# Kernel optimization log

Hardware: AMD Instinct MI355X
Metric: run time of the kernel (lower is better)

Reference implementation:

```python
import jax, jax.numpy as jnp
import numpy as np

B, C, H, W = 16, 1024, 32, 32  # H*W must equal C (required by matmul(h, fg) in the source)
EPS = 1e-5
NEG_SLOPE = 0.01


def setup_inputs() -> dict:
    key = jax.random.key(0)
    ks = jax.random.split(key, 12)
    s = 1.0 / np.sqrt(C)
    inp = {"x": jax.random.normal(ks[0], (B, C, H, W), jnp.float32)}
    for i, name in enumerate(["f", "g", "h", "c"]):
        inp[f"W{name}"] = jax.random.normal(ks[1 + 2 * i], (C, C), jnp.float32) * s
        inp[f"b{name}"] = jax.random.normal(ks[2 + 2 * i], (C,), jnp.float32) * 0.01
    inp["gamma"] = jnp.ones((C,), jnp.float32)
    inp["beta"] = jnp.zeros((C,), jnp.float32)
    inp["rmean"] = jax.random.normal(ks[9], (C,), jnp.float32) * 0.01
    inp["rvar"] = jax.random.uniform(ks[10], (C,), jnp.float32, 0.5, 1.5)
    return inp


def reference(x, Wf, bf, Wg, bg, Wh, bh, Wc, bc, gamma, beta, rmean, rvar):
    b, c, h_, w_ = x.shape
    n = h_ * w_  # == c by construction
    xf = x.reshape(b, c, n)

    def proj(Wp, bp):  # 1x1 conv == per-pixel channel matmul
        return jnp.einsum('oc,bcn->bon', Wp, xf) + bp[None, :, None]

    f = proj(Wf, bf)              # (B, C, N)
    g = proj(Wg, bg)              # (B, C, N); transposed(1,2) handled in einsum
    hh = proj(Wh, bh)             # (B, C, N)
    scores = jnp.einsum('bcn,bdn->bcd', f, g)        # f @ g^T -> (B, C, C)
    attn = jax.nn.softmax(scores, axis=1)            # softmax over dim=1 (as in source)
    # dropout2d(p=0.5) is identity in eval mode
    hfg = jnp.einsum('bcn,bnd->bcd', hh, attn)       # matmul(h, fg), needs N == C
    hfg = hfg.reshape(b, c, h_, w_)
    y = jnp.einsum('oc,bchw->bohw', Wc, hfg) + bc[None, :, None, None]
    y = jnp.where(y >= 0, y, NEG_SLOPE * y)          # LeakyReLU
    inv = gamma / jnp.sqrt(rvar + EPS)               # BatchNorm (eval mode)
    y = (y - rmean[None, :, None, None]) * inv[None, :, None, None] + beta[None, :, None, None]
    return y + x
```

## Files before the change

### kernel.cpp

```cpp
#include <hip/hip_runtime.h>
#include <cstdint>
#include <cstddef>

using half8  = __attribute__((ext_vector_type(8))) _Float16;
using half4  = __attribute__((ext_vector_type(4))) _Float16;
using float4v = __attribute__((ext_vector_type(4))) float;

#define CD 1024
#define M2 (1024 * 1024)

#define GLD16(gp, lp)                                                          \
    __builtin_amdgcn_global_load_lds(                                          \
        (const __attribute__((address_space(1))) void*)(gp),                   \
        (__attribute__((address_space(3))) void*)(lp), 16, 0, 0)

__global__ void prep_weights(const float* __restrict__ Wf, const float* __restrict__ Wg,
                             const float* __restrict__ Wh, const float* __restrict__ Wc,
                             const float* __restrict__ bf, const float* __restrict__ bg,
                             const float* __restrict__ bh,
                             _Float16* __restrict__ Wfgh, _Float16* __restrict__ WcH,
                             float* __restrict__ bstack) {
    int idx = blockIdx.x * 256 + threadIdx.x;
    if (idx < 3 * M2) {
        const float* s = idx < M2 ? Wf : (idx < 2 * M2 ? Wg : Wh);
        int off = idx & (M2 - 1);
        Wfgh[idx] = (_Float16)s[off];
    } else if (idx < 4 * M2) {
        WcH[idx - 3 * M2] = (_Float16)Wc[idx - 3 * M2];
    } else if (idx < 4 * M2 + 3 * CD) {
        int j = idx - 4 * M2;
        const float* s = j < CD ? bf : (j < 2 * CD ? bg : bh);
        bstack[j] = s[j & (CD - 1)];
    }
}

__global__ void transpose_x(const float* __restrict__ x, _Float16* __restrict__ xT, int b0) {
    __shared__ float tile[32][33];
    int z = blockIdx.z;
    const float* xb = x + (size_t)(b0 + z) * M2;
    _Float16* xTb = xT + (size_t)z * M2;
    int n0 = blockIdx.x * 32, k0 = blockIdx.y * 32;
    int tx = threadIdx.x, ty = threadIdx.y;
#pragma unroll
    for (int i = 0; i < 4; i++)
        tile[ty + i * 8][tx] = xb[(size_t)(k0 + ty + i * 8) * CD + n0 + tx];
    __syncthreads();
#pragma unroll
    for (int i = 0; i < 4; i++)
        xTb[(size_t)(n0 + ty + i * 8) * CD + k0 + tx] = (_Float16)tile[tx][ty + i * 8];
}

__global__ __launch_bounds__(256) void gemv_bch(const float* __restrict__ Wc,
                                                const float* __restrict__ bh,
                                                float* __restrict__ bch) {
    int o = blockIdx.x * 4 + (threadIdx.x >> 6);
    int lane = threadIdx.x & 63;
    float s = 0.f;
    for (int c = lane; c < CD; c += 64) s += Wc[(size_t)o * CD + c] * bh[c];
#pragma unroll
    for (int off = 32; off > 0; off >>= 1) s += __shfl_xor(s, off);
    if (lane == 0) bch[o] = s;
}

__global__ __launch_bounds__(256) void gemm128(const _Float16* __restrict__ A,
                                               const _Float16* __restrict__ B,
                                               _Float16* __restrict__ C) {
    __shared__ __align__(16) _Float16 As[128][32];
    __shared__ __align__(16) _Float16 Bs[128][32];
    int row0 = blockIdx.y * 128, col0 = blockIdx.x * 128;
    int tid = threadIdx.x, lane = tid & 63, wave = tid >> 6;
    int wr = wave >> 1, wc = wave & 1;
    const int srow = lane >> 2;
    const int scol = (lane & 3) * 8;
    const size_t gA0 = (size_t)(row0 + wave * 16 + srow) * 1024 + scol;
    const size_t gA1 = gA0 + (size_t)64 * 1024;
    const size_t gB0 = (size_t)(col0 + wave * 16 + srow) * 1024 + scol;
    const size_t gB1 = gB0 + (size_t)64 * 1024;
    _Float16* ldsA0 = &As[wave * 16][0];
    _Float16* ldsA1 = &As[64 + wave * 16][0];
    _Float16* ldsB0 = &Bs[wave * 16][0];
    _Float16* ldsB1 = &Bs[64 + wave * 16][0];
    float4v acc[4][4] = {};
    const int kq = (lane >> 4) * 8, rl = lane & 15;
    for (int kt = 0; kt < 1024; kt += 32) {
        GLD16(A + gA0 + kt, ldsA0);
        GLD16(A + gA1 + kt, ldsA1);
        GLD16(B + gB0 + kt, ldsB0);
        GLD16(B + gB1 + kt, ldsB1);
        __syncthreads();
        half8 af[4], bfr[4];
#pragma unroll
        for (int m = 0; m < 4; m++) af[m] = *(const half8*)(&As[wr * 64 + m * 16 + rl][kq]);
#pragma unroll
        for (int n = 0; n < 4; n++) bfr[n] = *(const half8*)(&Bs[wc * 64 + n * 16 + rl][kq]);
#pragma unroll
        for (int m = 0; m < 4; m++)
#pragma unroll
            for (int n = 0; n < 4; n++)
                acc[m][n] = __builtin_amdgcn_mfma_f32_16x16x32_f16(af[m], bfr[n], acc[m][n], 0, 0, 0);
        __syncthreads();
    }
#pragma unroll
    for (int m = 0; m < 4; m++)
#pragma unroll
        for (int r = 0; r < 4; r++) {
            int row = row0 + wr * 64 + m * 16 + ((lane >> 4) << 2) + r;
#pragma unroll
            for (int n = 0; n < 4; n++) {
                int col = col0 + wc * 64 + n * 16 + (lane & 15);
                C[(size_t)row * 1024 + col] = (_Float16)acc[m][n][r];
            }
        }
}

__global__ __launch_bounds__(256) void softmax_col(const float* __restrict__ ST,
                                                   _Float16* __restrict__ attnT) {
    int d = blockIdx.x, z = blockIdx.y;
    const float* row = ST + ((size_t)z * CD + d) * CD;
    _Float16* orow = attnT + ((size_t)z * CD + d) * CD;
    int t = threadIdx.x;
    float4v v = *(const float4v*)(row + t * 4);
    float mx = fmaxf(fmaxf(v[0], v[1]), fmaxf(v[2], v[3]));
#pragma unroll
    for (int o = 32; o > 0; o >>= 1) mx = fmaxf(mx, __shfl_xor(mx, o));
    __shared__ float redm[4], reds[4];
    int wave = t >> 6, lane = t & 63;
    if (lane == 0) redm[wave] = mx;
    __syncthreads();
    mx = fmaxf(fmaxf(redm[0], redm[1]), fmaxf(redm[2], redm[3]));
    float e[4];
    float s = 0.f;
#pragma unroll
    for (int i = 0; i < 4; i++) {
        e[i] = __expf(v[i] - mx);
        s += e[i];
    }
#pragma unroll
    for (int o = 32; o > 0; o >>= 1) s += __shfl_xor(s, o);
    if (lane == 0) reds[wave] = s;
    __syncthreads();
    s = reds[0] + reds[1] + reds[2] + reds[3];
    float inv = 1.0f / s;
    half4 ov;
#pragma unroll
    for (int i = 0; i < 4; i++) ov[i] = (_Float16)(e[i] * inv);
    *(half4*)(orow + t * 4) = ov;
}

enum { EP_F16B = 0, EP_F32 = 1, EP_F16 = 2, EP_FIN = 3 };

#define STAGE_A(T, BUF)                                                        \
    GLD16(gA0 + (size_t)(T) * 32, &As[BUF][wv * 16][0]);                       \
    GLD16(gA1 + (size_t)(T) * 32, &As[BUF][128 + wv * 16][0]);
#define STAGE_B(T, BUF)                                                        \
    GLD16(gB0 + (size_t)(T) * 32, &Bs[BUF][wv * 16][0]);                       \
    GLD16(gB1 + (size_t)(T) * 32, &Bs[BUF][128 + wv * 16][0]);

#define TILE(BUF, DOSTAGE, STT, STBUF, VMSTR)                                  \
    {                                                                          \
        asm volatile("s_waitcnt " VMSTR ::: "memory");                         \
        __builtin_amdgcn_sched_barrier(0);                                     \
        __builtin_amdgcn_s_barrier();                                          \
        _Pragma("unroll") for (int m = 0; m < 4; m++)                          \
            a[m] = *(const half8*)&As[BUF][wr * 128 + m * 16 + rl][kqa];       \
        _Pragma("unroll") for (int n = 0; n < 4; n++)                          \
            b[n] = *(const half8*)&Bs[BUF][wc * 64 + n * 16 + rl][kqa];        \
        _Pragma("unroll") for (int m = 4; m < 8; m++)                          \
            a[m] = *(const half8*)&As[BUF][wr * 128 + m * 16 + rl][kqa];       \
        if (DOSTAGE) { STAGE_A(STT, STBUF) STAGE_B(STT, STBUF) }               \
        __builtin_amdgcn_sched_barrier(0);                                     \
        __builtin_amdgcn_s_setprio(1);                                         \
        _Pragma("unroll") for (int m = 0; m < 8; m++)                          \
            _Pragma("unroll") for (int n = 0; n < 4; n++)                      \
                acc[m][n] = __builtin_amdgcn_mfma_f32_16x16x32_f16(            \
                    a[m], b[n], acc[m][n], 0, 0, 0);                           \
        __builtin_amdgcn_s_setprio(0);                                         \
    }

template <int EPI>
__global__ __launch_bounds__(512, 2) void gemm_nt(
    const _Float16* __restrict__ A, int64_t sA, const _Float16* __restrict__ B, int64_t sB,
    void* __restrict__ Cp, int64_t sC, const float* __restrict__ bias,
    const float* __restrict__ bc, const float* __restrict__ gamma,
    const float* __restrict__ beta, const float* __restrict__ rmean,
    const float* __restrict__ rvar, const float* __restrict__ xres) {
    __shared__ __align__(16) _Float16 As[4][256][32];
    __shared__ __align__(16) _Float16 Bs[4][256][32];
    int z = blockIdx.z;
    const _Float16* Ab = A + (size_t)z * sA;
    const _Float16* Bb = B + (size_t)z * sB;
    int row0 = blockIdx.y * 256, col0 = blockIdx.x * 256;
    int tid = threadIdx.x, lane = tid & 63, wv = tid >> 6;
    int wr = wv >> 2, wc = wv & 3;

    const int srow = wv * 16 + (lane >> 2);
    const int scol = ((lane & 3) ^ ((lane >> 3) & 3)) * 8;
    const _Float16* gA0 = Ab + (size_t)(row0 + srow) * 1024 + scol;
    const _Float16* gA1 = gA0 + (size_t)128 * 1024;
    const _Float16* gB0 = Bb + (size_t)(col0 + srow) * 1024 + scol;
    const _Float16* gB1 = gB0 + (size_t)128 * 1024;

    const int rl = lane & 15;
    const int kq = (lane >> 4) * 8;
    const int kqa = kq ^ (((rl >> 1) & 3) << 3);

    float4v acc[8][4] = {};
    half8 a[8], b[4];

    STAGE_A(0, 0) STAGE_B(0, 0)
    STAGE_A(1, 1) STAGE_B(1, 1)
    STAGE_A(2, 2) STAGE_B(2, 2)

#pragma unroll 1
    for (int g = 0; g < 7; ++g) {
        int t = g * 4;
        TILE(0, 1, t + 3, 3, "vmcnt(8)")
        TILE(1, 1, t + 4, 0, "vmcnt(8)")
        TILE(2, 1, t + 5, 1, "vmcnt(8)")
        TILE(3, 1, t + 6, 2, "vmcnt(8)")
    }
    TILE(0, 1, 31, 3, "vmcnt(8)")
    TILE(1, 0, 0, 0, "vmcnt(8)")
    TILE(2, 0, 0, 0, "vmcnt(4)")
    TILE(3, 0, 0, 0, "vmcnt(0)")

#pragma unroll
    for (int m = 0; m < 8; m++) {
#pragma unroll
        for (int r = 0; r < 4; r++) {
            int row = row0 + wr * 128 + m * 16 + ((lane >> 4) << 2) + r;
            float add0 = 0.f, mu = 0.f, invs = 1.f, bet = 0.f;
            if constexpr (EPI == EP_F16B) add0 = bias[row];
            if constexpr (EPI == EP_FIN) {
                add0 = bc[row];
                mu = rmean[row];
                invs = gamma[row] * rsqrtf(rvar[row] + 1e-5f);
                bet = beta[row];
            }
#pragma unroll
            for (int n = 0; n < 4; n++) {
                int col = col0 + wc * 64 + n * 16 + (lane & 15);
                float v = acc[m][n][r];
                if constexpr (EPI == EP_F16B) {
                    ((_Float16*)Cp)[(size_t)z * sC + (size_t)row * 1024 + col] = (_Float16)(v + add0);
                } else if constexpr (EPI == EP_F32) {
                    ((float*)Cp)[(size_t)z * sC + (size_t)row * 1024 + col] = v;
                } else if constexpr (EPI == EP_F16) {
                    ((_Float16*)Cp)[(size_t)z * sC + (size_t)row * 1024 + col] = (_Float16)v;
                } else {
                    v += add0;
                    v = v >= 0.f ? v : 0.01f * v;
                    v = (v - mu) * invs + bet;
                    v += xres[(size_t)z * M2 + (size_t)row * 1024 + col];
                    ((float*)Cp)[(size_t)z * sC + (size_t)row * 1024 + col] = v;
                }
            }
        }
    }
}

extern "C" void kernel_launch(void* const* d_in, const int* in_sizes, int n_in,
                              void* d_out, int out_size, void* d_ws, size_t ws_size,
                              hipStream_t stream) {
    const float* x = (const float*)d_in[0];
    const float* Wf = (const float*)d_in[1];
    const float* bf = (const float*)d_in[2];
    const float* Wg = (const float*)d_in[3];
    const float* bg = (const float*)d_in[4];
    const float* Wh = (const float*)d_in[5];
    const float* bh = (const float*)d_in[6];
    const float* Wc = (const float*)d_in[7];
    const float* bc = (const float*)d_in[8];
    const float* gamma = (const float*)d_in[9];
    const float* beta = (const float*)d_in[10];
    const float* rmean = (const float*)d_in[11];
    const float* rvar = (const float*)d_in[12];

    char* p = (char*)d_ws;
    _Float16* Wfgh = (_Float16*)p;
    p += (size_t)3 * M2 * 2;
    _Float16* WcH = (_Float16*)p;
    p += (size_t)M2 * 2;
    float* bstack = (float*)p;
    p += (size_t)3 * CD * 4;
    size_t fixed = (size_t)(p - (char*)d_ws);
    fixed = (fixed + 255) & ~(size_t)255;

    size_t perB = (size_t)2 * M2 + (size_t)6 * M2 + (size_t)4 * M2;
    int nb = 16;
    while (nb > 1 && fixed + (size_t)nb * perB > ws_size) nb >>= 1;

    char* q = (char*)d_ws + fixed;

    {
        int total = 4 * M2 + 3 * CD;
        prep_weights<<<dim3((total + 255) / 256), dim3(256), 0, stream>>>(
            Wf, Wg, Wh, Wc, bf, bg, bh, Wfgh, WcH, bstack);
    }
    {
        _Float16* WhT = (_Float16*)q;
        transpose_x<<<dim3(32, 32, 1), dim3(32, 8), 0, stream>>>(Wh, WhT, 0);
        gemv_bch<<<dim3(256), dim3(256), 0, stream>>>(Wc, bh, bstack + 2 * CD);
        gemm128<<<dim3(8, 8), dim3(256), 0, stream>>>(WcH, WhT, Wfgh + (size_t)2 * M2);
    }

    for (int b0 = 0; b0 < 16; b0 += nb) {
        _Float16* xT = (_Float16*)q;
        _Float16* FGH = (_Float16*)(q + (size_t)nb * 2 * M2);
        float* ST = (float*)(q + (size_t)nb * 8 * M2);
        _Float16* attnT = xT;

        transpose_x<<<dim3(32, 32, nb), dim3(32, 8), 0, stream>>>(x, xT, b0);
        gemm_nt<EP_F16B><<<dim3(4, 12, nb), dim3(512), 0, stream>>>(
            Wfgh, 0, xT, M2, FGH, (int64_t)3 * M2, bstack,
            nullptr, nullptr, nullptr, nullptr, nullptr, nullptr);
        gemm_nt<EP_F32><<<dim3(4, 4, nb), dim3(512), 0, stream>>>(
            FGH + M2, (int64_t)3 * M2, FGH, (int64_t)3 * M2, ST, M2,
            nullptr, nullptr, nullptr, nullptr, nullptr, nullptr, nullptr);
        softmax_col<<<dim3(1024, nb), dim3(256), 0, stream>>>(ST, attnT);
        gemm_nt<EP_FIN><<<dim3(4, 4, nb), dim3(512), 0, stream>>>(
            FGH + (size_t)2 * M2, (int64_t)3 * M2, attnT, M2,
            (float*)d_out + (size_t)b0 * M2, M2,
            nullptr, bc, gamma, beta, rmean, rvar, x + (size_t)b0 * M2);
    }
}
```

Baseline: 290.7 us.

## Restructure GEMM mainloop to 64-wide K tiles with double buffering and quarter-phase interleave

```diff
diff --git a/kernel.cpp b/kernel.cpp
--- a/kernel.cpp
+++ b/kernel.cpp
@@ -149,32 +149,66 @@
 
 enum { EP_F16B = 0, EP_F32 = 1, EP_F16 = 2, EP_FIN = 3 };
 
-#define STAGE_A(T, BUF)                                                        \
-    GLD16(gA0 + (size_t)(T) * 32, &As[BUF][wv * 16][0]);                       \
-    GLD16(gA1 + (size_t)(T) * 32, &As[BUF][128 + wv * 16][0]);
-#define STAGE_B(T, BUF)                                                        \
-    GLD16(gB0 + (size_t)(T) * 32, &Bs[BUF][wv * 16][0]);                       \
-    GLD16(gB1 + (size_t)(T) * 32, &Bs[BUF][128 + wv * 16][0]);
-
-#define TILE(BUF, DOSTAGE, STT, STBUF, VMSTR)                                  \
-    {                                                                          \
-        asm volatile("s_waitcnt " VMSTR ::: "memory");                         \
-        __builtin_amdgcn_sched_barrier(0);                                     \
-        __builtin_amdgcn_s_barrier();                                          \
-        _Pragma("unroll") for (int m = 0; m < 4; m++)                          \
-            a[m] = *(const half8*)&As[BUF][wr * 128 + m * 16 + rl][kqa];       \
-        _Pragma("unroll") for (int n = 0; n < 4; n++)                          \
-            b[n] = *(const half8*)&Bs[BUF][wc * 64 + n * 16 + rl][kqa];        \
-        _Pragma("unroll") for (int m = 4; m < 8; m++)                          \
-            a[m] = *(const half8*)&As[BUF][wr * 128 + m * 16 + rl][kqa];       \
-        if (DOSTAGE) { STAGE_A(STT, STBUF) STAGE_B(STT, STBUF) }               \
-        __builtin_amdgcn_sched_barrier(0);                                     \
-        __builtin_amdgcn_s_setprio(1);                                         \
-        _Pragma("unroll") for (int m = 0; m < 8; m++)                          \
-            _Pragma("unroll") for (int n = 0; n < 4; n++)                      \
-                acc[m][n] = __builtin_amdgcn_mfma_f32_16x16x32_f16(            \
-                    a[m], b[n], acc[m][n], 0, 0, 0);                           \
-        __builtin_amdgcn_s_setprio(0);                                         \
+#define SBAR0 __builtin_amdgcn_sched_barrier(0);
+#define PBAR __builtin_amdgcn_s_barrier();
+
+#define STG_A(T, HALF, BUF)                                                    \
+    GLD16(gA + (size_t)((HALF) * 128 + 0) * 1024 + (T) * 64,                   \
+          &As[BUF][(HALF) * 128 + wv * 16 + 0][0]);                            \
+    GLD16(gA + (size_t)((HALF) * 128 + 8) * 1024 + (T) * 64,                   \
+          &As[BUF][(HALF) * 128 + wv * 16 + 8][0]);
+#define STG_B(T, HALF, BUF)                                                    \
+    GLD16(gB + (size_t)((HALF) * 128 + 0) * 1024 + (T) * 64,                   \
+          &Bs[BUF][(HALF) * 128 + wv * 16 + 0][0]);                            \
+    GLD16(gB + (size_t)((HALF) * 128 + 8) * 1024 + (T) * 64,                   \
+          &Bs[BUF][(HALF) * 128 + wv * 16 + 8][0]);
+
+#define RD_A(MB, BUF)                                                          \
+    _Pragma("unroll") for (int i = 0; i < 4; i++)                              \
+        _Pragma("unroll") for (int ks = 0; ks < 2; ks++)                       \
+            a[i][ks] = *(const half8*)&As[BUF][wr * 128 + ((MB) + i) * 16 + rl][col8[ks]];
+#define RD_B(N0, BUF)                                                          \
+    _Pragma("unroll") for (int n = 0; n < 2; n++)                              \
+        _Pragma("unroll") for (int ks = 0; ks < 2; ks++)                       \
+            b[(N0) + n][ks] = *(const half8*)&Bs[BUF][wc * 64 + ((N0) + n) * 16 + rl][col8[ks]];
+
+#define MF_Q(MB, NB)                                                           \
+    __builtin_amdgcn_s_setprio(1);                                             \
+    _Pragma("unroll") for (int i = 0; i < 4; i++)                              \
+        _Pragma("unroll") for (int nn = 0; nn < 2; nn++) {                     \
+            acc[(MB) + i][(NB) + nn] = __builtin_amdgcn_mfma_f32_16x16x32_f16( \
+                a[i][0], b[(NB) + nn][0], acc[(MB) + i][(NB) + nn], 0, 0, 0);  \
+            acc[(MB) + i][(NB) + nn] = __builtin_amdgcn_mfma_f32_16x16x32_f16( \
+                a[i][1], b[(NB) + nn][1], acc[(MB) + i][(NB) + nn], 0, 0, 0);  \
+        }                                                                      \
+    __builtin_amdgcn_s_setprio(0);
+
+#define TILE64(BUF, OBUF, SA, TA, SB, TB, DOVM, VMSTR, LAST)                   \
+    {                                                                  \
+        RD_A(0, BUF) RD_B(0, BUF)                                              \
+        if (SA) { STG_A(TA, 0, OBUF) }                                         \
+        asm volatile("s_waitcnt lgkmcnt(8)" ::: "memory"); SBAR0               \
+        PBAR                                                                   \
+        asm volatile("s_waitcnt lgkmcnt(0)" ::: "memory"); SBAR0               \
+        MF_Q(0, 0) PBAR                                                        \
+                                                                       \
+        RD_B(2, BUF)                                                           \
+        if (SA) { STG_A(TA, 1, OBUF) }                                         \
+        PBAR                                                                   \
+        asm volatile("s_waitcnt lgkmcnt(0)" ::: "memory"); SBAR0               \
+        MF_Q(0, 2) PBAR                                                        \
+                                                                       \
+        RD_A(4, BUF)                                                           \
+        if (SB) { STG_B(TB, 0, BUF) }                                          \
+        PBAR                                                                   \
+        asm volatile("s_waitcnt lgkmcnt(0)" ::: "memory"); SBAR0               \
+        MF_Q(4, 0) PBAR                                                        \
+                                                                       \
+        if (SB) { STG_B(TB, 1, BUF) }                                          \
+        if (!(LAST)) { PBAR }                                                  \
+        MF_Q(4, 2)                                                             \
+        if (DOVM) { asm volatile("s_waitcnt " VMSTR ::: "memory"); SBAR0 }     \
+        if (!(LAST)) { PBAR }                                                  \
     }
 
 template <int EPI>
@@ -184,8 +218,8 @@
     const float* __restrict__ bc, const float* __restrict__ gamma,
     const float* __restrict__ beta, const float* __restrict__ rmean,
     const float* __restrict__ rvar, const float* __restrict__ xres) {
-    __shared__ __align__(16) _Float16 As[4][256][32];
-    __shared__ __align__(16) _Float16 Bs[4][256][32];
+    __shared__ __align__(16) _Float16 As[2][256][64];
+    __shared__ __align__(16) _Float16 Bs[2][256][64];
     int z = blockIdx.z;
     const _Float16* Ab = A + (size_t)z * sA;
     const _Float16* Bb = B + (size_t)z * sB;
@@ -193,36 +227,34 @@
     int tid = threadIdx.x, lane = tid & 63, wv = tid >> 6;
     int wr = wv >> 2, wc = wv & 3;
 
-    const int srow = wv * 16 + (lane >> 2);
-    const int scol = ((lane & 3) ^ ((lane >> 3) & 3)) * 8;
-    const _Float16* gA0 = Ab + (size_t)(row0 + srow) * 1024 + scol;
-    const _Float16* gA1 = gA0 + (size_t)128 * 1024;
-    const _Float16* gB0 = Bb + (size_t)(col0 + srow) * 1024 + scol;
-    const _Float16* gB1 = gB0 + (size_t)128 * 1024;
+    const _Float16* gA = Ab + (size_t)(row0 + wv * 16 + (lane >> 3)) * 1024 +
+                         ((lane & 7) ^ (lane >> 3)) * 8;
+    const _Float16* gB = Bb + (size_t)(col0 + wv * 16 + (lane >> 3)) * 1024 +
+                         ((lane & 7) ^ (lane >> 3)) * 8;
 
     const int rl = lane & 15;
-    const int kq = (lane >> 4) * 8;
-    const int kqa = kq ^ (((rl >> 1) & 3) << 3);
+    const int col8[2] = {(((lane >> 4)) ^ (rl & 7)) * 8,
+                         (((lane >> 4) + 4) ^ (rl & 7)) * 8};
 
     float4v acc[8][4] = {};
-    half8 a[8], b[4];
-
-    STAGE_A(0, 0) STAGE_B(0, 0)
-    STAGE_A(1, 1) STAGE_B(1, 1)
-    STAGE_A(2, 2) STAGE_B(2, 2)
-
+    half8 a[4][2], b[4][2];
+
+    STG_A(0, 0, 0) STG_A(0, 1, 0) STG_B(0, 0, 0) STG_B(0, 1, 0)
+    STG_A(1, 0, 1) STG_A(1, 1, 1) STG_B(1, 0, 1) STG_B(1, 1, 1)
+    asm volatile("s_waitcnt vmcnt(8)" ::: "memory");
+    SBAR0
+    PBAR
+
+    TILE64(0, 1, 0, 0, 1, 2, 1, "vmcnt(4)", 0)
+    TILE64(1, 0, 1, 2, 1, 3, 1, "vmcnt(4)", 0)
 #pragma unroll 1
-    for (int g = 0; g < 7; ++g) {
-        int t = g * 4;
-        TILE(0, 1, t + 3, 3, "vmcnt(8)")
-        TILE(1, 1, t + 4, 0, "vmcnt(8)")
-        TILE(2, 1, t + 5, 1, "vmcnt(8)")
-        TILE(3, 1, t + 6, 2, "vmcnt(8)")
-    }
-    TILE(0, 1, 31, 3, "vmcnt(8)")
-    TILE(1, 0, 0, 0, "vmcnt(8)")
-    TILE(2, 0, 0, 0, "vmcnt(4)")
-    TILE(3, 0, 0, 0, "vmcnt(0)")
+    for (int g = 1; g < 7; ++g) {
+        int t = 2 * g;
+        TILE64(0, 1, 1, t + 1, 1, t + 2, 1, "vmcnt(4)", 0)
+        TILE64(1, 0, 1, t + 2, 1, t + 3, 1, "vmcnt(4)", 0)
+    }
+    TILE64(0, 1, 1, 15, 0, 0, 1, "vmcnt(0)", 0)
+    TILE64(1, 0, 0, 0, 0, 0, 0, "", 1)
 
 #pragma unroll
     for (int m = 0; m < 8; m++) {
```

Measured after the change: 305.9 us. +5.2%, slower.

## Switch GEMM mainloop to double-buffered 64-wide K tiles with split staging

Applied to the files above, without the earlier changes.

```diff
diff --git a/kernel.cpp b/kernel.cpp
--- a/kernel.cpp
+++ b/kernel.cpp
@@ -149,32 +149,42 @@
 
 enum { EP_F16B = 0, EP_F32 = 1, EP_F16 = 2, EP_FIN = 3 };
 
-#define STAGE_A(T, BUF)                                                        \
-    GLD16(gA0 + (size_t)(T) * 32, &As[BUF][wv * 16][0]);                       \
-    GLD16(gA1 + (size_t)(T) * 32, &As[BUF][128 + wv * 16][0]);
-#define STAGE_B(T, BUF)                                                        \
-    GLD16(gB0 + (size_t)(T) * 32, &Bs[BUF][wv * 16][0]);                       \
-    GLD16(gB1 + (size_t)(T) * 32, &Bs[BUF][128 + wv * 16][0]);
-
-#define TILE(BUF, DOSTAGE, STT, STBUF, VMSTR)                                  \
+#define STG_A(T, BUF)                                                          \
+    GLD16(gA + (size_t)(T) * 64 + 0 * 8192, &As[BUF][wv * 32 + 0][0]);         \
+    GLD16(gA + (size_t)(T) * 64 + 1 * 8192, &As[BUF][wv * 32 + 8][0]);         \
+    GLD16(gA + (size_t)(T) * 64 + 2 * 8192, &As[BUF][wv * 32 + 16][0]);        \
+    GLD16(gA + (size_t)(T) * 64 + 3 * 8192, &As[BUF][wv * 32 + 24][0]);
+#define STG_B(T, BUF)                                                          \
+    GLD16(gB + (size_t)(T) * 64 + 0 * 8192, &Bs[BUF][wv * 32 + 0][0]);         \
+    GLD16(gB + (size_t)(T) * 64 + 1 * 8192, &Bs[BUF][wv * 32 + 8][0]);         \
+    GLD16(gB + (size_t)(T) * 64 + 2 * 8192, &Bs[BUF][wv * 32 + 16][0]);        \
+    GLD16(gB + (size_t)(T) * 64 + 3 * 8192, &Bs[BUF][wv * 32 + 24][0]);
+
+#define READS(SET, BUF, COL)                                                   \
+    _Pragma("unroll") for (int m = 0; m < 8; m++)                              \
+        a##SET[m] = *(const half8*)&As[BUF][wr * 128 + m * 16 + rl][COL];      \
+    _Pragma("unroll") for (int n = 0; n < 4; n++)                              \
+        b##SET[n] = *(const half8*)&Bs[BUF][wc * 64 + n * 16 + rl][COL];
+
+#define MFMA32(SET)                                                            \
+    __builtin_amdgcn_s_setprio(1);                                             \
+    _Pragma("unroll") for (int m = 0; m < 8; m++)                              \
+        _Pragma("unroll") for (int n = 0; n < 4; n++)                          \
+            acc[m][n] = __builtin_amdgcn_mfma_f32_16x16x32_f16(                \
+                a##SET[m], b##SET[n], acc[m][n], 0, 0, 0);                     \
+    __builtin_amdgcn_s_setprio(0);
+
+#define TILE64(BUF, OBUF, DOSTAGE, STT)                                        \
     {                                                                          \
-        asm volatile("s_waitcnt " VMSTR ::: "memory");                         \
+        asm volatile("s_waitcnt vmcnt(0)" ::: "memory");                       \
         __builtin_amdgcn_sched_barrier(0);                                     \
         __builtin_amdgcn_s_barrier();                                          \
-        _Pragma("unroll") for (int m = 0; m < 4; m++)                          \
-            a[m] = *(const half8*)&As[BUF][wr * 128 + m * 16 + rl][kqa];       \
-        _Pragma("unroll") for (int n = 0; n < 4; n++)                          \
-            b[n] = *(const half8*)&Bs[BUF][wc * 64 + n * 16 + rl][kqa];        \
-        _Pragma("unroll") for (int m = 4; m < 8; m++)                          \
-            a[m] = *(const half8*)&As[BUF][wr * 128 + m * 16 + rl][kqa];       \
-        if (DOSTAGE) { STAGE_A(STT, STBUF) STAGE_B(STT, STBUF) }               \
-        __builtin_amdgcn_sched_barrier(0);                                     \
-        __builtin_amdgcn_s_setprio(1);                                         \
-        _Pragma("unroll") for (int m = 0; m < 8; m++)                          \
-            _Pragma("unroll") for (int n = 0; n < 4; n++)                      \
-                acc[m][n] = __builtin_amdgcn_mfma_f32_16x16x32_f16(            \
-                    a[m], b[n], acc[m][n], 0, 0, 0);                           \
-        __builtin_amdgcn_s_setprio(0);                                         \
+        READS(0, BUF, c0)                                                      \
+        if (DOSTAGE) { STG_A(STT, OBUF) }                                      \
+        MFMA32(0)                                                              \
+        READS(1, BUF, c1)                                                      \
+        if (DOSTAGE) { STG_B(STT, OBUF) }                                      \
+        MFMA32(1)                                                              \
     }
 
 template <int EPI>
@@ -184,8 +194,8 @@
     const float* __restrict__ bc, const float* __restrict__ gamma,
     const float* __restrict__ beta, const float* __restrict__ rmean,
     const float* __restrict__ rvar, const float* __restrict__ xres) {
-    __shared__ __align__(16) _Float16 As[4][256][32];
-    __shared__ __align__(16) _Float16 Bs[4][256][32];
+    __shared__ __align__(16) _Float16 As[2][256][64];
+    __shared__ __align__(16) _Float16 Bs[2][256][64];
     int z = blockIdx.z;
     const _Float16* Ab = A + (size_t)z * sA;
     const _Float16* Bb = B + (size_t)z * sB;
@@ -193,36 +203,29 @@
     int tid = threadIdx.x, lane = tid & 63, wv = tid >> 6;
     int wr = wv >> 2, wc = wv & 3;
 
-    const int srow = wv * 16 + (lane >> 2);
-    const int scol = ((lane & 3) ^ ((lane >> 3) & 3)) * 8;
-    const _Float16* gA0 = Ab + (size_t)(row0 + srow) * 1024 + scol;
-    const _Float16* gA1 = gA0 + (size_t)128 * 1024;
-    const _Float16* gB0 = Bb + (size_t)(col0 + srow) * 1024 + scol;
-    const _Float16* gB1 = gB0 + (size_t)128 * 1024;
+    const _Float16* gA = Ab + (size_t)(row0 + wv * 32 + (lane >> 3)) * 1024 +
+                         ((lane & 7) ^ (lane >> 3)) * 8;
+    const _Float16* gB = Bb + (size_t)(col0 + wv * 32 + (lane >> 3)) * 1024 +
+                         ((lane & 7) ^ (lane >> 3)) * 8;
 
     const int rl = lane & 15;
-    const int kq = (lane >> 4) * 8;
-    const int kqa = kq ^ (((rl >> 1) & 3) << 3);
+    const int q = lane >> 4;
+    const int c0 = ((q) ^ (rl & 7)) * 8;
+    const int c1 = ((q + 4) ^ (rl & 7)) * 8;
 
     float4v acc[8][4] = {};
-    half8 a[8], b[4];
-
-    STAGE_A(0, 0) STAGE_B(0, 0)
-    STAGE_A(1, 1) STAGE_B(1, 1)
-    STAGE_A(2, 2) STAGE_B(2, 2)
+    half8 a0[8], b0[4], a1[8], b1[4];
+
+    STG_A(0, 0) STG_B(0, 0)
 
 #pragma unroll 1
     for (int g = 0; g < 7; ++g) {
-        int t = g * 4;
-        TILE(0, 1, t + 3, 3, "vmcnt(8)")
-        TILE(1, 1, t + 4, 0, "vmcnt(8)")
-        TILE(2, 1, t + 5, 1, "vmcnt(8)")
-        TILE(3, 1, t + 6, 2, "vmcnt(8)")
-    }
-    TILE(0, 1, 31, 3, "vmcnt(8)")
-    TILE(1, 0, 0, 0, "vmcnt(8)")
-    TILE(2, 0, 0, 0, "vmcnt(4)")
-    TILE(3, 0, 0, 0, "vmcnt(0)")
+        int t = 2 * g;
+        TILE64(0, 1, 1, t + 1)
+        TILE64(1, 0, 1, t + 2)
+    }
+    TILE64(0, 1, 1, 15)
+    TILE64(1, 0, 0, 0)
 
 #pragma unroll
     for (int m = 0; m < 8; m++) {
```

Result: faster. 279.3 us (-3.9%).
